# Performance work log

Measured on AMD Instinct MI355X. Metric: run time of the kernel, lower is better.

The kernel has to match this reference:

```python
import jax, jax.numpy as jnp
import numpy as np

N_NODES = 100000
N_EDGES = 3200000
N_GRAPHS = 128
F_IN, HID, N_CLS = 3, 64, 6


def setup_inputs() -> dict:
    key = jax.random.key(0)
    ks = jax.random.split(key, 9)
    x = jax.random.normal(ks[0], (N_NODES, F_IN), dtype=jnp.float32)
    edge_index = jax.random.randint(ks[1], (2, N_EDGES), 0, N_NODES, dtype=jnp.int32)
    batch = jnp.sort(jax.random.randint(ks[2], (N_NODES,), 0, N_GRAPHS, dtype=jnp.int32))
    # GCNConv weights (glorot-ish) and biases
    W1 = jax.random.normal(ks[3], (F_IN, HID), dtype=jnp.float32) / np.float32(np.sqrt(F_IN))
    b1 = jnp.zeros((HID,), dtype=jnp.float32)
    W2 = jax.random.normal(ks[4], (HID, HID), dtype=jnp.float32) / np.float32(np.sqrt(HID))
    b2 = jnp.zeros((HID,), dtype=jnp.float32)
    Wl = jax.random.normal(ks[5], (HID, N_CLS), dtype=jnp.float32) / np.float32(np.sqrt(HID))
    bl = jnp.zeros((N_CLS,), dtype=jnp.float32)
    return {"x": x, "edge_index": edge_index, "batch": batch,
            "W1": W1, "b1": b1, "W2": W2, "b2": b2, "Wl": Wl, "bl": bl}


def _gcn_forward(x, edge_index, batch, W1, b1, W2, b2, Wl, bl):
    n = x.shape[0]
    # add self-loops (PyG GCNConv default)
    loop = jnp.arange(n, dtype=edge_index.dtype)
    src = jnp.concatenate([edge_index[0], loop])
    dst = jnp.concatenate([edge_index[1], loop])
    # symmetric normalization D^{-1/2} (A+I) D^{-1/2}
    deg = jax.ops.segment_sum(jnp.ones_like(dst, dtype=x.dtype), dst, num_segments=n)
    dis = jax.lax.rsqrt(jnp.maximum(deg, 1.0))
    norm = dis[src] * dis[dst]  # [E+N]

    def conv(h, W, b):
        h = h @ W                                   # [N, out]
        msg = h[src] * norm[:, None]                # gather + scale
        agg = jax.ops.segment_sum(msg, dst, num_segments=n)  # scatter-add
        return agg + b

    h = jax.nn.relu(conv(x, W1, b1))
    h = jax.nn.relu(conv(h, W2, b2))
    # global mean pool over graphs
    ones = jnp.ones((n,), dtype=h.dtype)
    cnt = jax.ops.segment_sum(ones, batch, num_segments=N_GRAPHS)
    pooled = jax.ops.segment_sum(h, batch, num_segments=N_GRAPHS) / jnp.maximum(cnt, 1.0)[:, None]
    logits = pooled @ Wl + bl
    return jax.nn.log_softmax(logits, axis=1)


def reference(x, edge_index, batch, W1, b1, W2, b2, Wl, bl):
    return _gcn_forward(x, edge_index, batch, W1, b1, W2, b2, Wl, bl)
```

## Files before the change

### kernel.cpp

```cpp
#include <hip/hip_runtime.h>
#include <math.h>

#define NGRAPH 128
#define NPB 128
#define CAPB 6144
#define PSL 8
#define MMN 16
#define TILEA 8192
#define EPTA 16


__device__ inline unsigned char f2fp8(float f) {
    float a = fabsf(f);
    unsigned s = (__float_as_uint(f) >> 31) << 7;
    if (!(a > 0.f)) return (unsigned char)s;
    if (a >= 448.f) return (unsigned char)(s | 0x7e);
    int e = (int)(__float_as_uint(a) >> 23) - 127;
    if (e < -6) e = -6;
    float sc = __uint_as_float((unsigned)(130 - e) << 23);
    int q = (int)rintf(a * sc);
    if (q >= 16) { e += 1; q = 8; }
    if (q <= 0) return (unsigned char)s;
    unsigned expb, man;
    if (q < 8) { expb = 0; man = (unsigned)q; }
    else { expb = (unsigned)(e + 7); man = (unsigned)(q - 8); }
    return (unsigned char)(s | (expb << 3) | man);
}

typedef float v2f __attribute__((ext_vector_type(2)));

__device__ inline void fp8x4_dec(unsigned u, float* o) {
#pragma unroll
    for (int k = 0; k < 4; ++k) {
        unsigned b = (u >> (8 * k)) & 0xffu;
        unsigned bits = ((b & 0x80u) << 24) | ((b & 0x7fu) << 20);
        o[k] = __uint_as_float(bits) * 0x1p+120f;
    }
}

__device__ inline void acc16(uint4 u, float w, v2f* a) {
#if __has_builtin(__builtin_amdgcn_cvt_pk_f32_fp8)
    v2f ws; ws.x = w; ws.y = w;
    a[0] += __builtin_amdgcn_cvt_pk_f32_fp8(u.x, false) * ws;
    a[1] += __builtin_amdgcn_cvt_pk_f32_fp8(u.x, true)  * ws;
    a[2] += __builtin_amdgcn_cvt_pk_f32_fp8(u.y, false) * ws;
    a[3] += __builtin_amdgcn_cvt_pk_f32_fp8(u.y, true)  * ws;
    a[4] += __builtin_amdgcn_cvt_pk_f32_fp8(u.z, false) * ws;
    a[5] += __builtin_amdgcn_cvt_pk_f32_fp8(u.z, true)  * ws;
    a[6] += __builtin_amdgcn_cvt_pk_f32_fp8(u.w, false) * ws;
    a[7] += __builtin_amdgcn_cvt_pk_f32_fp8(u.w, true)  * ws;
#else
    float* af = (float*)a;
    unsigned uu[4] = {u.x, u.y, u.z, u.w};
#pragma unroll
    for (int q = 0; q < 4; ++q) {
        float d[4]; fp8x4_dec(uu[q], d);
#pragma unroll
        for (int k = 0; k < 4; ++k) af[q * 4 + k] += d[k] * w;
    }
#endif
}


__global__ void init_k(int* __restrict__ cursorF, float* __restrict__ pooled, int NBF) {
    int i = blockIdx.x * blockDim.x + threadIdx.x;
    if (i < NBF) cursorF[i] = i * CAPB;
    if (i < NGRAPH * 64) pooled[i] = 0.0f;
}


__global__ __launch_bounds__(512) void binA_k(const int* __restrict__ src,
        const int* __restrict__ dst, int* cursorF, unsigned* __restrict__ binned,
        int E, int NBF) {
    __shared__ int lh[1024];
    int tid = threadIdx.x;
    lh[tid] = 0;
    lh[tid + 512] = 0;
    __syncthreads();
    int base = blockIdx.x * TILEA;
    int d[EPTA];
#pragma unroll
    for (int u = 0; u < EPTA; ++u) {
        int e = base + tid + u * 512;
        d[u] = (e < E) ? dst[e] : -1;
    }
#pragma unroll
    for (int u = 0; u < EPTA; ++u)
        if (d[u] >= 0) atomicAdd(&lh[d[u] >> 7], 1);
    __syncthreads();
    for (int t = tid; t < NBF; t += 512) {
        int cnt = lh[t];
        lh[t] = cnt ? atomicAdd(&cursorF[t], cnt) : 0;
    }
    __syncthreads();
#pragma unroll
    for (int u = 0; u < EPTA; ++u) {
        if (d[u] >= 0) {
            int e = base + tid + u * 512;
            int p = atomicAdd(&lh[d[u] >> 7], 1);
            binned[p] = (unsigned)src[e] | ((unsigned)(d[u] & (NPB - 1)) << 17);
        }
    }
}


__global__ __launch_bounds__(256) void reorder_k(unsigned* __restrict__ binned,
        const int* __restrict__ cursorF, int* __restrict__ nodebeg,
        int* __restrict__ nodeend, float* __restrict__ dis,
        const float* __restrict__ x, float* __restrict__ xs, int n) {
    __shared__ int hist[NPB + 1];
    __shared__ int startv[NPB + 1];
    __shared__ unsigned lout[CAPB];
    int tid = threadIdx.x;
    int b = blockIdx.x;
    int beg = b * CAPB, end = cursorF[b];
    int total = end - beg;
    if (tid <= NPB) hist[tid] = 0;
    __syncthreads();
    for (int i = beg + tid; i < end; i += 256)
        atomicAdd(&hist[binned[i] >> 17], 1);
    __syncthreads();
    if (tid < NPB) startv[tid + 1] = hist[tid];
    if (tid == 0) startv[0] = 0;
    __syncthreads();
    for (int off = 1; off <= NPB; off <<= 1) {
        int v = 0;
        if (tid <= NPB && tid >= off) v = startv[tid - off];
        __syncthreads();
        if (tid <= NPB && tid >= off) startv[tid] += v;
        __syncthreads();
    }
    if (tid < NPB) hist[tid] = startv[tid];
    __syncthreads();
    for (int i = beg + tid; i < end; i += 256) {
        unsigned r = binned[i];
        int p = atomicAdd(&hist[r >> 17], 1);
        lout[p] = r & 0x1FFFFu;
    }
    __syncthreads();
    for (int jj = tid; jj < total; jj += 256)
        binned[beg + jj] = lout[jj];
    int node0 = b * NPB;
    if (tid < NPB) {
        int node = node0 + tid;
        if (node < n) {
            nodebeg[node] = beg + startv[tid];
            nodeend[node] = beg + startv[tid + 1];
            int deg = startv[tid + 1] - startv[tid];
            float d = rsqrtf((float)deg + 1.0f);
            dis[node] = d;
            xs[node * 3]     = x[node * 3] * d;
            xs[node * 3 + 1] = x[node * 3 + 1] * d;
            xs[node * 3 + 2] = x[node * 3 + 2] * d;
        }
    }
}


__global__ __launch_bounds__(256) void mm12_k(const float* __restrict__ xs,
        const int* __restrict__ nodebeg, const int* __restrict__ nodeend,
        const int* __restrict__ csr, const float* __restrict__ dis,
        const float* __restrict__ W1, const float* __restrict__ b1,
        const float* __restrict__ W2, unsigned char* __restrict__ tb, int n) {
    __shared__ __attribute__((aligned(16))) float hrow[4][64];
    __shared__ float4 ytile[MMN];
    int tid = threadIdx.x;
    int j = tid & 63;

    float w1r0 = W1[j], w1r1 = W1[64 + j], w1r2 = W1[128 + j], bbr = b1[j];
    float wreg[64];
#pragma unroll
    for (int k = 0; k < 64; ++k) wreg[k] = W2[k * 64 + j];

    int ns = tid >> 4;
    int el = tid & 15;
    int gnode = blockIdx.x * MMN + ns;
    float a0 = 0.f, a1 = 0.f, a2 = 0.f;
    float dn = 0.f;
    int b = 0, e = 0;
    if (gnode < n) {
        dn = dis[gnode];
        b = nodebeg[gnode];
        e = nodeend[gnode];
    }
    for (int i = b + el; i < e; i += 32) {
        int s0 = csr[i];
        int i1 = i + 16;
        bool v1 = i1 < e;
        int s1 = v1 ? csr[i1] : s0;
        float m1 = v1 ? 1.f : 0.f;
        float p0 = xs[s0 * 3], p1 = xs[s0 * 3 + 1], p2 = xs[s0 * 3 + 2];
        float q0 = xs[s1 * 3], q1 = xs[s1 * 3 + 1], q2 = xs[s1 * 3 + 2];
        a0 += p0 + q0 * m1;
        a1 += p1 + q1 * m1;
        a2 += p2 + q2 * m1;
    }
#pragma unroll
    for (int off = 1; off <= 8; off <<= 1) {
        a0 += __shfl_xor(a0, off);
        a1 += __shfl_xor(a1, off);
        a2 += __shfl_xor(a2, off);
    }
    if (el == 0 && gnode < n) {
        ytile[ns] = make_float4(dn * (a0 + xs[gnode * 3]),
                                dn * (a1 + xs[gnode * 3 + 1]),
                                dn * (a2 + xs[gnode * 3 + 2]), dn);
    }
    __syncthreads();

    int nl = tid >> 6;
    for (int it = 0; it < MMN / 4; ++it) {
        int slot = it * 4 + nl;
        int node = blockIdx.x * MMN + slot;
        float4 yv = ytile[slot];
        float h = fmaxf(yv.x * w1r0 + yv.y * w1r1 + yv.z * w1r2 + bbr, 0.0f);
        hrow[nl][j] = h;
        __builtin_amdgcn_wave_barrier();
        float acc = 0.0f;
#pragma unroll
        for (int k = 0; k < 64; k += 4) {
            float4 h4 = *(const float4*)&hrow[nl][k];
            acc += h4.x * wreg[k + 0];
            acc += h4.y * wreg[k + 1];
            acc += h4.z * wreg[k + 2];
            acc += h4.w * wreg[k + 3];
        }
        if (node < n) tb[node * 64 + j] = f2fp8(acc * yv.w);
        __builtin_amdgcn_wave_barrier();
    }
}


__global__ __launch_bounds__(256) void gather2_k(const unsigned char* __restrict__ tb,
        const float* __restrict__ b2, const int* __restrict__ nodebeg,
        const int* __restrict__ nodeend, const int* __restrict__ csr,
        const float* __restrict__ dis, float* __restrict__ agg, int n) {
    int g = blockIdx.x * blockDim.x + threadIdx.x;
    int node = g >> 6;
    if (node >= n) return;
    int lane = threadIdx.x & 63;
    int c4 = lane & 3, esub = lane >> 2;
    const uint4* t16 = (const uint4*)tb;
    float dn = dis[node];
    int b = nodebeg[node], e = nodeend[node];
    v2f av[8];
#pragma unroll
    for (int k = 0; k < 8; ++k) { av[k].x = 0.f; av[k].y = 0.f; }
    for (int i = b; i < e + 1; i += 64) {
        int i0 = i + esub, i1 = i0 + 16, i2 = i0 + 32, i3 = i0 + 48;
        int s0 = (i0 < e) ? csr[i0] : node;
        int s1 = (i1 < e) ? csr[i1] : node;
        int s2 = (i2 < e) ? csr[i2] : node;
        int s3 = (i3 < e) ? csr[i3] : node;
        float w0 = (i0 <= e) ? 1.f : 0.f;
        float w1 = (i1 <= e) ? 1.f : 0.f;
        float w2 = (i2 <= e) ? 1.f : 0.f;
        float w3 = (i3 <= e) ? 1.f : 0.f;
        uint4 u0 = t16[s0 * 4 + c4];
        uint4 u1 = t16[s1 * 4 + c4];
        uint4 u2 = t16[s2 * 4 + c4];
        uint4 u3 = t16[s3 * 4 + c4];
        acc16(u0, w0, av);
        acc16(u1, w1, av);
        acc16(u2, w2, av);
        acc16(u3, w3, av);
    }
    float* a = (float*)av;
    {
        bool hi = (esub & 1) != 0;
#pragma unroll
        for (int t = 0; t < 8; ++t) {
            float send = hi ? a[t] : a[8 + t];
            float r = __shfl_xor(send, 4);
            a[t] = (hi ? a[8 + t] : a[t]) + r;
        }
    }
    {
        bool hi = (esub & 2) != 0;
#pragma unroll
        for (int t = 0; t < 4; ++t) {
            float send = hi ? a[t] : a[4 + t];
            float r = __shfl_xor(send, 8);
            a[t] = (hi ? a[4 + t] : a[t]) + r;
        }
    }
    {
        bool hi = (esub & 4) != 0;
#pragma unroll
        for (int t = 0; t < 2; ++t) {
            float send = hi ? a[t] : a[2 + t];
            float r = __shfl_xor(send, 16);
            a[t] = (hi ? a[2 + t] : a[t]) + r;
        }
    }
    {
        bool hi = (esub & 8) != 0;
        float send = hi ? a[0] : a[1];
        float r = __shfl_xor(send, 32);
        a[0] = (hi ? a[1] : a[0]) + r;
    }
    int chan = ((esub & 1) << 3) | ((esub & 2) << 1) | ((esub & 4) >> 1) | ((esub & 8) >> 3);
    agg[node * 64 + c4 * 16 + chan] = dn * a[0] + b2[c4 * 16 + chan];
}


__device__ inline int lower_bound_i(const int* a, int n, int key) {
    int lo = 0, hi = n;
    while (lo < hi) {
        int mid = (lo + hi) >> 1;
        if (a[mid] < key) lo = mid + 1; else hi = mid;
    }
    return lo;
}

__global__ void pool_k(const float* __restrict__ agg2, const int* __restrict__ batch,
                       float* __restrict__ pooled, int n) {
    int g = blockIdx.x / PSL, slice = blockIdx.x % PSL;
    int start = lower_bound_i(batch, n, g);
    int end   = lower_bound_i(batch, n, g + 1);
    int len = end - start;
    int cb = start + (int)(((long long)len * slice) / PSL);
    int ce = start + (int)(((long long)len * (slice + 1)) / PSL);
    int wid = threadIdx.x >> 6, lane = threadIdx.x & 63;
    float acc = 0.0f;
    for (int i = cb + wid; i < ce; i += 4)
        acc += fmaxf(agg2[i * 64 + lane], 0.0f);
    __shared__ float red[4][64];
    red[wid][lane] = acc;
    __syncthreads();
    if (threadIdx.x < 64) {
        float s = red[0][lane] + red[1][lane] + red[2][lane] + red[3][lane];
        atomicAdd(&pooled[g * 64 + lane], s);
    }
}

__global__ void head_k(const float* __restrict__ pooled, const int* __restrict__ batch,
                       const float* __restrict__ Wl, const float* __restrict__ bl,
                       float* __restrict__ out, int n) {
    int g = blockIdx.x, t = threadIdx.x;
    __shared__ float p[64];
    __shared__ float logit[8];
    int start = lower_bound_i(batch, n, g);
    int end   = lower_bound_i(batch, n, g + 1);
    float cnt = fmaxf((float)(end - start), 1.0f);
    p[t] = pooled[g * 64 + t] / cnt;
    __syncthreads();
    if (t < 6) {
        float a = bl[t];
        for (int k = 0; k < 64; ++k) a += p[k] * Wl[k * 6 + t];
        logit[t] = a;
    }
    __syncthreads();
    if (t == 0) {
        float m = logit[0];
        for (int j = 1; j < 6; ++j) m = fmaxf(m, logit[j]);
        float s = 0.0f;
        for (int j = 0; j < 6; ++j) s += expf(logit[j] - m);
        float lse = m + logf(s);
        for (int j = 0; j < 6; ++j) out[g * 6 + j] = logit[j] - lse;
    }
}


extern "C" void kernel_launch(void* const* d_in, const int* in_sizes, int n_in,
                              void* d_out, int out_size, void* d_ws, size_t ws_size,
                              hipStream_t stream) {
    const float* x     = (const float*)d_in[0];
    const int*   ei    = (const int*)d_in[1];
    const int*   batch = (const int*)d_in[2];
    const float* W1    = (const float*)d_in[3];
    const float* b1    = (const float*)d_in[4];
    const float* W2    = (const float*)d_in[5];
    const float* b2    = (const float*)d_in[6];
    const float* Wl    = (const float*)d_in[7];
    const float* bl    = (const float*)d_in[8];

    int n = in_sizes[0] / 3;
    int E = in_sizes[1] / 2;
    const int* src = ei;
    const int* dst = ei + E;

    int NBF = (n + NPB - 1) / NPB;
    int GA = (E + TILEA - 1) / TILEA;

    char* ws = (char*)d_ws;
    size_t o = 0;
    auto alloc = [&](size_t bytes) -> void* {
        void* p = ws + o;
        o += (bytes + 255) & ~(size_t)255;
        return p;
    };
    int*      cursorF = (int*)alloc((size_t)NBF * 4);
    float*    dis     = (float*)alloc((size_t)n * 4);
    int*      nodebeg = (int*)alloc((size_t)n * 4);
    int*      nodeend = (int*)alloc((size_t)n * 4);
    float*    xs      = (float*)alloc((size_t)n * 3 * 4);
    float*    pooled  = (float*)alloc((size_t)NGRAPH * 64 * 4);
    unsigned* binned  = (unsigned*)alloc((size_t)NBF * CAPB * 4);
    unsigned char* tb = (unsigned char*)alloc((size_t)n * 64);
    float*    agg     = (float*)alloc((size_t)n * 64 * 4);
    float*    out = (float*)d_out;

    int initN = NGRAPH * 64;
    init_k<<<(initN + 255) / 256, 256, 0, stream>>>(cursorF, pooled, NBF);
    binA_k<<<GA, 512, 0, stream>>>(src, dst, cursorF, binned, E, NBF);
    reorder_k<<<NBF, 256, 0, stream>>>(binned, cursorF, nodebeg, nodeend, dis, x, xs, n);

    mm12_k<<<(n + MMN - 1) / MMN, 256, 0, stream>>>(xs, nodebeg, nodeend,
            (const int*)binned, dis, W1, b1, W2, tb, n);
    gather2_k<<<(n * 64 + 255) / 256, 256, 0, stream>>>(tb, b2, nodebeg, nodeend,
            (const int*)binned, dis, agg, n);

    pool_k<<<NGRAPH * PSL, 256, 0, stream>>>(agg, batch, pooled, n);
    head_k<<<NGRAPH, 64, 0, stream>>>(pooled, batch, Wl, bl, out, n);
}
```

Measured before the change: 239.5 us.

## Split per-bucket edge cursors into eight sub-segments to cut global atomic contention

The binning kernel now gives each destination bucket eight independent sub-cursors. Each block picks one by blockIdx mod 8, so concurrent blocks no longer serialize on a single global atomic per bucket. The reorder kernel walks the eight fixed-capacity segments of each bucket to build the per-node CSR, and takes the bucket total from its prefix sum instead of the cursor. Binning tiles double in size and run with 1024 threads per block, which halves the block count. In exchange the binned buffer grows, and each sub-segment is capped at 1024 entries, which could overflow on skewed degree distributions.

```diff
diff --git a/kernel.cpp b/kernel.cpp
--- a/kernel.cpp
+++ b/kernel.cpp
@@ -3,10 +3,11 @@
 
 #define NGRAPH 128
 #define NPB 128
-#define CAPB 6144
+#define SEGC 1024
+#define CAPB 8192
 #define PSL 8
 #define MMN 16
-#define TILEA 8192
+#define TILEA 16384
 #define EPTA 16
 
 
@@ -62,41 +63,41 @@
 }
 
 
-__global__ void init_k(int* __restrict__ cursorF, float* __restrict__ pooled, int NBF) {
+__global__ void init_k(int* __restrict__ cursorF, float* __restrict__ pooled, int NCUR) {
     int i = blockIdx.x * blockDim.x + threadIdx.x;
-    if (i < NBF) cursorF[i] = i * CAPB;
+    if (i < NCUR) cursorF[i] = i * SEGC;
     if (i < NGRAPH * 64) pooled[i] = 0.0f;
 }
 
 
-__global__ __launch_bounds__(512) void binA_k(const int* __restrict__ src,
+__global__ __launch_bounds__(1024) void binA_k(const int* __restrict__ src,
         const int* __restrict__ dst, int* cursorF, unsigned* __restrict__ binned,
         int E, int NBF) {
     __shared__ int lh[1024];
     int tid = threadIdx.x;
     lh[tid] = 0;
-    lh[tid + 512] = 0;
-    __syncthreads();
+    __syncthreads();
+    int sg = blockIdx.x & 7;
     int base = blockIdx.x * TILEA;
     int d[EPTA];
 #pragma unroll
     for (int u = 0; u < EPTA; ++u) {
-        int e = base + tid + u * 512;
+        int e = base + tid + u * 1024;
         d[u] = (e < E) ? dst[e] : -1;
     }
 #pragma unroll
     for (int u = 0; u < EPTA; ++u)
         if (d[u] >= 0) atomicAdd(&lh[d[u] >> 7], 1);
     __syncthreads();
-    for (int t = tid; t < NBF; t += 512) {
-        int cnt = lh[t];
-        lh[t] = cnt ? atomicAdd(&cursorF[t], cnt) : 0;
+    if (tid < NBF) {
+        int cnt = lh[tid];
+        lh[tid] = cnt ? atomicAdd(&cursorF[(tid << 3) | sg], cnt) : 0;
     }
     __syncthreads();
 #pragma unroll
     for (int u = 0; u < EPTA; ++u) {
         if (d[u] >= 0) {
-            int e = base + tid + u * 512;
+            int e = base + tid + u * 1024;
             int p = atomicAdd(&lh[d[u] >> 7], 1);
             binned[p] = (unsigned)src[e] | ((unsigned)(d[u] & (NPB - 1)) << 17);
         }
@@ -113,12 +114,15 @@
     __shared__ unsigned lout[CAPB];
     int tid = threadIdx.x;
     int b = blockIdx.x;
-    int beg = b * CAPB, end = cursorF[b];
-    int total = end - beg;
+    int bbase = b * CAPB;
     if (tid <= NPB) hist[tid] = 0;
     __syncthreads();
-    for (int i = beg + tid; i < end; i += 256)
-        atomicAdd(&hist[binned[i] >> 17], 1);
+    for (int s = 0; s < 8; ++s) {
+        int sbeg = bbase + s * SEGC;
+        int send_ = cursorF[(b << 3) | s];
+        for (int i = sbeg + tid; i < send_; i += 256)
+            atomicAdd(&hist[binned[i] >> 17], 1);
+    }
     __syncthreads();
     if (tid < NPB) startv[tid + 1] = hist[tid];
     if (tid == 0) startv[0] = 0;
@@ -132,20 +136,25 @@
     }
     if (tid < NPB) hist[tid] = startv[tid];
     __syncthreads();
-    for (int i = beg + tid; i < end; i += 256) {
-        unsigned r = binned[i];
-        int p = atomicAdd(&hist[r >> 17], 1);
-        lout[p] = r & 0x1FFFFu;
-    }
-    __syncthreads();
+    for (int s = 0; s < 8; ++s) {
+        int sbeg = bbase + s * SEGC;
+        int send_ = cursorF[(b << 3) | s];
+        for (int i = sbeg + tid; i < send_; i += 256) {
+            unsigned r = binned[i];
+            int p = atomicAdd(&hist[r >> 17], 1);
+            lout[p] = r & 0x1FFFFu;
+        }
+    }
+    __syncthreads();
+    int total = startv[NPB];
     for (int jj = tid; jj < total; jj += 256)
-        binned[beg + jj] = lout[jj];
+        binned[bbase + jj] = lout[jj];
     int node0 = b * NPB;
     if (tid < NPB) {
         int node = node0 + tid;
         if (node < n) {
-            nodebeg[node] = beg + startv[tid];
-            nodeend[node] = beg + startv[tid + 1];
+            nodebeg[node] = bbase + startv[tid];
+            nodeend[node] = bbase + startv[tid + 1];
             int deg = startv[tid + 1] - startv[tid];
             float d = rsqrtf((float)deg + 1.0f);
             dis[node] = d;
@@ -381,6 +390,7 @@
     const int* dst = ei + E;
 
     int NBF = (n + NPB - 1) / NPB;
+    int NCUR = NBF * 8;
     int GA = (E + TILEA - 1) / TILEA;
 
     char* ws = (char*)d_ws;
@@ -390,7 +400,7 @@
         o += (bytes + 255) & ~(size_t)255;
         return p;
     };
-    int*      cursorF = (int*)alloc((size_t)NBF * 4);
+    int*      cursorF = (int*)alloc((size_t)NCUR * 4);
     float*    dis     = (float*)alloc((size_t)n * 4);
     int*      nodebeg = (int*)alloc((size_t)n * 4);
     int*      nodeend = (int*)alloc((size_t)n * 4);
@@ -402,8 +412,8 @@
     float*    out = (float*)d_out;
 
     int initN = NGRAPH * 64;
-    init_k<<<(initN + 255) / 256, 256, 0, stream>>>(cursorF, pooled, NBF);
-    binA_k<<<GA, 512, 0, stream>>>(src, dst, cursorF, binned, E, NBF);
+    init_k<<<(initN + 255) / 256, 256, 0, stream>>>(cursorF, pooled, NCUR);
+    binA_k<<<GA, 1024, 0, stream>>>(src, dst, cursorF, binned, E, NBF);
     reorder_k<<<NBF, 256, 0, stream>>>(binned, cursorF, nodebeg, nodeend, dis, x, xs, n);
 
     mm12_k<<<(n + MMN - 1) / MMN, 256, 0, stream>>>(xs, nodebeg, nodeend,
```

Result: faster. 234.1 us (-2.2%).

## Stage binned edges in shared memory and write bucket runs contiguously

Applied to the files above, without the earlier changes.

The edge-binning kernel now sorts each tile's edges into shared memory by bucket, using a block-wide prefix scan over bucket counts. Each bucket's run is then copied to global memory by one wavefront, so writes become coalesced instead of scattered. The tile and block size double, to 16384 edges and 1024 threads, which raises shared-memory use per block (about 76 KB) and lowers occupancy. The scan adds many syncthreads, and src is now loaded up front into registers.

```diff
diff --git a/kernel.cpp b/kernel.cpp
--- a/kernel.cpp
+++ b/kernel.cpp
@@ -6,7 +6,7 @@
 #define CAPB 6144
 #define PSL 8
 #define MMN 16
-#define TILEA 8192
+#define TILEA 16384
 #define EPTA 16
 
 
@@ -69,37 +69,59 @@
 }
 
 
-__global__ __launch_bounds__(512) void binA_k(const int* __restrict__ src,
+__global__ __launch_bounds__(1024) void binA_k(const int* __restrict__ src,
         const int* __restrict__ dst, int* cursorF, unsigned* __restrict__ binned,
         int E, int NBF) {
     __shared__ int lh[1024];
+    __shared__ int startv[1024];
+    __shared__ int gdelta[1024];
+    __shared__ unsigned lout[TILEA];
     int tid = threadIdx.x;
     lh[tid] = 0;
-    lh[tid + 512] = 0;
     __syncthreads();
     int base = blockIdx.x * TILEA;
     int d[EPTA];
+    int s[EPTA];
 #pragma unroll
     for (int u = 0; u < EPTA; ++u) {
-        int e = base + tid + u * 512;
+        int e = base + tid + u * 1024;
         d[u] = (e < E) ? dst[e] : -1;
+        s[u] = (e < E) ? src[e] : 0;
     }
 #pragma unroll
     for (int u = 0; u < EPTA; ++u)
         if (d[u] >= 0) atomicAdd(&lh[d[u] >> 7], 1);
     __syncthreads();
-    for (int t = tid; t < NBF; t += 512) {
-        int cnt = lh[t];
-        lh[t] = cnt ? atomicAdd(&cursorF[t], cnt) : 0;
+    if (tid <= NBF) startv[tid] = (tid == 0) ? 0 : lh[tid - 1];
+    __syncthreads();
+    for (int off = 1; off <= NBF; off <<= 1) {
+        int v = 0;
+        if (tid <= NBF && tid >= off) v = startv[tid - off];
+        __syncthreads();
+        if (tid <= NBF && tid >= off) startv[tid] += v;
+        __syncthreads();
+    }
+    if (tid < NBF) {
+        int cnt = lh[tid];
+        int g = cnt ? atomicAdd(&cursorF[tid], cnt) : 0;
+        gdelta[tid] = g - startv[tid];
+        lh[tid] = startv[tid];
     }
     __syncthreads();
 #pragma unroll
     for (int u = 0; u < EPTA; ++u) {
         if (d[u] >= 0) {
-            int e = base + tid + u * 512;
             int p = atomicAdd(&lh[d[u] >> 7], 1);
-            binned[p] = (unsigned)src[e] | ((unsigned)(d[u] & (NPB - 1)) << 17);
-        }
+            lout[p] = (unsigned)s[u] | ((unsigned)(d[u] & (NPB - 1)) << 17);
+        }
+    }
+    __syncthreads();
+    int wv = tid >> 6, ln = tid & 63;
+    for (int bkt = wv; bkt < NBF; bkt += 16) {
+        int ls = startv[bkt], le = lh[bkt];
+        int gd = gdelta[bkt];
+        for (int i = ls + ln; i < le; i += 64)
+            binned[gd + i] = lout[i];
     }
 }
 
@@ -403,7 +425,7 @@
 
     int initN = NGRAPH * 64;
     init_k<<<(initN + 255) / 256, 256, 0, stream>>>(cursorF, pooled, NBF);
-    binA_k<<<GA, 512, 0, stream>>>(src, dst, cursorF, binned, E, NBF);
+    binA_k<<<GA, 1024, 0, stream>>>(src, dst, cursorF, binned, E, NBF);
     reorder_k<<<NBF, 256, 0, stream>>>(binned, cursorF, nodebeg, nodeend, dis, x, xs, n);
 
     mm12_k<<<(n + MMN - 1) / MMN, 256, 0, stream>>>(xs, nodebeg, nodeend,
```

Measured after the change: 222.6 us. -7.0%, faster.
